# Kernel optimization log

Hardware: AMD Instinct MI355X
Metric: run time of the kernel (lower is better)

Reference implementation:

```python
import jax, jax.numpy as jnp
import numpy as np
from jax import lax


def setup_inputs() -> dict:
    key = jax.random.key(0)
    kx, kw = jax.random.split(key)
    x = jax.random.normal(kx, (32, 3, 8192), dtype=jnp.float32)
    weight = jax.random.normal(kw, (128, 3, 64), dtype=jnp.float32)
    return {"x": x, "weight": weight}


def reference(x, weight):
    # x: [B, C, L], weight: [O, C, K]
    K = weight.shape[2]
    # Cross-correlation (conv1d, no bias, valid padding): [B, O, L-K+1]
    conv_out = lax.conv_general_dilated(
        x, weight, window_strides=(1,), padding='VALID',
        dimension_numbers=('NCH', 'OIH', 'NCH'))
    # Half squared norm of each shapelet: [O]
    w_norm = jnp.sum(weight ** 2, axis=(1, 2)) / 2
    # Half squared norm of each length-K window, via cumulative sums
    # (avoids materializing the [B, C, W, K] unfold tensor)
    sq = jnp.sum(x ** 2, axis=1)               # [B, L]
    c = jnp.pad(jnp.cumsum(sq, axis=1), ((0, 0), (1, 0)))  # [B, L+1]
    win_norm = (c[:, K:] - c[:, :-K]) / 2      # [B, L-K+1]
    # features = conv_out - (||w||^2/2 + ||window||^2/2)
    features = conv_out - w_norm[None, :, None] - win_norm[:, None, :]
    # global max-pool over time, then *(-2) -> min squared distance
    return -2.0 * jnp.max(features, axis=-1)   # [B, O]
```

## Files before the change

kernel.cpp:

```cpp
#include <hip/hip_runtime.h>
#include <float.h>

#define BB 32
#define LL 8192
#define OO 128
#define KK 64
#define WW (LL - KK + 1)
#define TC 32

typedef __attribute__((ext_vector_type(8))) short short8;
typedef __attribute__((ext_vector_type(4))) float f32x4;

union AB { int4 i4; int i[4]; short8 v; };
union AB2 { struct { int4 a, b; } p; int i[8]; };

static __device__ __forceinline__ unsigned int f2bf(float f) {
    unsigned int u = __builtin_bit_cast(unsigned int, f);
    return (u + 0x7FFFu + ((u >> 16) & 1u)) >> 16;
}

__global__ __launch_bounds__(256) void prep_kernel(const float* __restrict__ w,
                                                   unsigned short* __restrict__ wswz,
                                                   float* __restrict__ wn) {
    int g = blockIdx.x * 256 + threadIdx.x;
    if (g < 3072) {
        int ob = (g >= 1536) ? 1 : 0;
        int gg = g - ob * 1536;
        int ksqp = gg >> 6;
        int o2   = gg & 63;
        int ks = ksqp >> 2, qp = ksqp & 3;
        int c = ks >> 1, h = ks & 1;
        const float4* p = (const float4*)(w + (ob * 64 + o2) * 192 + c * 64 + h * 32 + qp * 8);
        float4 v0 = p[0], v1 = p[1];
        int4 pk;
        pk.x = (int)(f2bf(v0.x) | (f2bf(v0.y) << 16));
        pk.y = (int)(f2bf(v0.z) | (f2bf(v0.w) << 16));
        pk.z = (int)(f2bf(v1.x) | (f2bf(v1.y) << 16));
        pk.w = (int)(f2bf(v1.z) | (f2bf(v1.w) << 16));
        ((int4*)wswz)[g] = pk;
    }
    int oo = g - 3072;
    if (oo >= 0 && oo < OO) {
        const float* p = w + oo * 192;
        float s = 0.f;
        for (int i = 0; i < 192; ++i) { float v = p[i]; s = fmaf(v, v, s); }
        wn[oo] = 0.5f * s;
    }
}

__global__ __launch_bounds__(256, 3) void shapeconv_main(const float* __restrict__ x,
                                                         const unsigned short* __restrict__ wswz,
                                                         const float* __restrict__ wn,
                                                         float* __restrict__ partial) {
    __shared__ __align__(16) unsigned short w_lds[64 * 192];
    __shared__ __align__(16) unsigned short x_lds[3 * 320];
    __shared__ float sq_lds[320];
    __shared__ float P_lds[40];
    __shared__ float win_lds[272];
    __shared__ float wn_lds[64];
    __shared__ float mred[64];

    const int tc = blockIdx.x;
    const int ob = blockIdx.y;
    const int b  = blockIdx.z;
    const int tid = threadIdx.x;
    const int wv = tid >> 6;
    const int lane = tid & 63;
    const int wo = wv & 1, wt = wv >> 1;
    const int n  = lane & 15;
    const int qp = lane >> 4;
    const int T0 = tc * 256;

    {
        const char* src = (const char*)(wswz + ob * 1536 * 8) + tid * 16;
        #pragma unroll
        for (int i = 0; i < 6; ++i) {
            __builtin_amdgcn_global_load_lds(
                (const __attribute__((address_space(1))) unsigned int*)(src + i * 4096),
                (__attribute__((address_space(3))) unsigned int*)((char*)w_lds + wv * 1024 + i * 4096),
                16, 0, 0);
        }
    }
    if (tid < 64) wn_lds[tid] = wn[ob * 64 + tid];

    if (tid < 240) {
        int c = tid / 80, j4 = tid - c * 80;
        int l = T0 + j4 * 4;
        float4 v = make_float4(0.f, 0.f, 0.f, 0.f);
        if (l < LL) v = *(const float4*)(x + (b * 3 + c) * LL + l);
        uint2 pk;
        pk.x = f2bf(v.x) | (f2bf(v.y) << 16);
        pk.y = f2bf(v.z) | (f2bf(v.w) << 16);
        *(uint2*)(x_lds + c * 320 + j4 * 4) = pk;
    }
    for (int j = tid; j < 320; j += 256) {
        int l = T0 + j;
        float s = 0.f;
        if (l < LL) {
            #pragma unroll
            for (int c = 0; c < 3; ++c) {
                float v = x[(b * 3 + c) * LL + l];
                s = fmaf(v, v, s);
            }
        }
        sq_lds[j] = s;
    }
    if (tid < 40) {
        float s = 0.f;
        #pragma unroll
        for (int k = 0; k < 8; ++k) {
            int l = T0 + tid * 8 + k;
            if (l < LL) {
                #pragma unroll
                for (int c = 0; c < 3; ++c) {
                    float v = x[(b * 3 + c) * LL + l];
                    s = fmaf(v, v, s);
                }
            }
        }
        P_lds[tid] = s;
    }
    __syncthreads();

    {
        int a = tid >> 3, bb2 = tid & 7;
        float s = 0.f;
        #pragma unroll
        for (int i = 1; i <= 7; ++i) s += P_lds[a + i];
        #pragma unroll
        for (int k = 0; k < 8; ++k)
            s += (k >= bb2) ? sq_lds[8 * a + k] : sq_lds[8 * a + 64 + k];
        int pi = tid + (tid >> 4);
        win_lds[pi] = (T0 + tid < WW) ? 0.5f * s : 1e30f;
    }
    __syncthreads();

    f32x4 acc[2][8];
    {
        float wl[8];
        #pragma unroll
        for (int r = 0; r < 8; ++r) {
            int tl = 128 * wt + r + 8 * n;
            wl[r] = win_lds[tl + (tl >> 4)];
        }
        #pragma unroll
        for (int ot = 0; ot < 2; ++ot)
            #pragma unroll
            for (int rg = 0; rg < 4; ++rg) {
                float nw = wn_lds[32 * wo + 16 * ot + 4 * qp + rg];
                #pragma unroll
                for (int r = 0; r < 8; ++r)
                    acc[ot][r][rg] = -nw - wl[r];
            }
    }

    const char* xb = (const char*)x_lds;
    #pragma unroll
    for (int ks = 0; ks < 6; ++ks) {
        int c = ks >> 1, h = ks & 1;
        int e0b = c * 640 + 256 * wt + 64 * h + 16 * (n + qp);
        AB2 D;
        D.p.a = *(const int4*)(xb + e0b);
        D.p.b = *(const int4*)(xb + e0b + 16);
        AB a0, a1;
        const int4* wq = (const int4*)w_lds + (ks * 4 + qp) * 64 + 32 * wo;
        a0.i4 = wq[n];
        a1.i4 = wq[16 + n];
        #pragma unroll
        for (int r = 0; r < 8; ++r) {
            AB bf;
            int s = r >> 1;
            if ((r & 1) == 0) {
                bf.i[0] = D.i[s]; bf.i[1] = D.i[s + 1]; bf.i[2] = D.i[s + 2]; bf.i[3] = D.i[s + 3];
            } else {
                #pragma unroll
                for (int d = 0; d < 4; ++d)
                    bf.i[d] = (int)(((unsigned)D.i[s + d] >> 16) | ((unsigned)D.i[s + d + 1] << 16));
            }
            acc[0][r] = __builtin_amdgcn_mfma_f32_16x16x32_bf16(a0.v, bf.v, acc[0][r], 0, 0, 0);
            acc[1][r] = __builtin_amdgcn_mfma_f32_16x16x32_bf16(a1.v, bf.v, acc[1][r], 0, 0, 0);
        }
    }

    float m2[2][4];
    #pragma unroll
    for (int ot = 0; ot < 2; ++ot)
        #pragma unroll
        for (int rg = 0; rg < 4; ++rg) {
            float mm = acc[ot][0][rg];
            #pragma unroll
            for (int r = 1; r < 8; ++r) mm = fmaxf(mm, acc[ot][r][rg]);
            m2[ot][rg] = mm;
        }
    #pragma unroll
    for (int s = 1; s <= 8; s <<= 1)
        #pragma unroll
        for (int ot = 0; ot < 2; ++ot)
            #pragma unroll
            for (int rg = 0; rg < 4; ++rg)
                m2[ot][rg] = fmaxf(m2[ot][rg], __shfl_xor(m2[ot][rg], s, 64));

    if (wt == 1 && n == 0) {
        #pragma unroll
        for (int ot = 0; ot < 2; ++ot)
            #pragma unroll
            for (int rg = 0; rg < 4; ++rg)
                mred[32 * wo + 16 * ot + 4 * qp + rg] = m2[ot][rg];
    }
    __syncthreads();
    if (wt == 0 && n == 0) {
        #pragma unroll
        for (int ot = 0; ot < 2; ++ot)
            #pragma unroll
            for (int rg = 0; rg < 4; ++rg) {
                int oi = 32 * wo + 16 * ot + 4 * qp + rg;
                float v = fmaxf(m2[ot][rg], mred[oi]);
                partial[((size_t)(b * TC + tc) * 2 + ob) * 64 + oi] = v;
            }
    }
}

__global__ __launch_bounds__(256) void reduce_kernel(const float* __restrict__ partial,
                                                     float* __restrict__ out) {
    int idx = blockIdx.x * 256 + threadIdx.x;
    int b = idx >> 7, o = idx & 127;
    const float* pp = partial + ((size_t)b * TC * 2 + (o >> 6)) * 64 + (o & 63);
    float mx = -FLT_MAX;
    #pragma unroll 8
    for (int tcc = 0; tcc < TC; ++tcc) mx = fmaxf(mx, pp[(size_t)tcc * 128]);
    out[idx] = -2.f * mx;
}

extern "C" void kernel_launch(void* const* d_in, const int* in_sizes, int n_in,
                              void* d_out, int out_size, void* d_ws, size_t ws_size,
                              hipStream_t stream) {
    const float* x = (const float*)d_in[0];
    const float* w = (const float*)d_in[1];
    float* out = (float*)d_out;

    unsigned short* wswz = (unsigned short*)d_ws;
    float* wn = (float*)((char*)d_ws + 49152);
    float* partial = (float*)((char*)d_ws + 49664);

    prep_kernel<<<13, 256, 0, stream>>>(w, wswz, wn);
    dim3 grid(TC, 2, BB);
    shapeconv_main<<<grid, 256, 0, stream>>>(x, wswz, wn, partial);
    reduce_kernel<<<16, 256, 0, stream>>>(partial, out);
}
```

Before: 82.64 us.

## Process four time chunks per block with double-buffered x staging

Each block now loops over four 256-sample time chunks instead of one. This amortizes the 24KB weight load into LDS across more work and cuts the grid from 2048 to 512 blocks. The next chunk's x data is staged into a second LDS buffer while the current chunk runs its MFMAs. The 8-sample partial sums are now computed with warp shuffles instead of redundant global reads. The risks are lower occupancy (launch bounds 2), fewer blocks to fill the GPU, and extra barriers per chunk.

```diff
diff --git a/kernel.cpp b/kernel.cpp
--- a/kernel.cpp
+++ b/kernel.cpp
@@ -6,13 +6,13 @@
 #define OO 128
 #define KK 64
 #define WW (LL - KK + 1)
-#define TC 32
+#define NCH 4
+#define GX 8
 
 typedef __attribute__((ext_vector_type(8))) short short8;
 typedef __attribute__((ext_vector_type(4))) float f32x4;
 
 union AB { int4 i4; int i[4]; short8 v; };
-union AB2 { struct { int4 a, b; } p; int i[8]; };
 
 static __device__ __forceinline__ unsigned int f2bf(float f) {
     unsigned int u = __builtin_bit_cast(unsigned int, f);
@@ -48,19 +48,66 @@
     }
 }
 
-__global__ __launch_bounds__(256, 3) void shapeconv_main(const float* __restrict__ x,
+static __device__ __forceinline__ void stage_chunk(const float* __restrict__ x, int b, int T0,
+                                                   unsigned short* xl, float* sql, float* Pl,
+                                                   int tid) {
+    if (tid < 240) {
+        int c = tid / 80, j4 = tid - c * 80;
+        int l = T0 + j4 * 4;
+        float4 v = make_float4(0.f, 0.f, 0.f, 0.f);
+        if (l < LL) v = *(const float4*)(x + (b * 3 + c) * LL + l);
+        uint2 pk;
+        pk.x = f2bf(v.x) | (f2bf(v.y) << 16);
+        pk.y = f2bf(v.z) | (f2bf(v.w) << 16);
+        *(uint2*)(xl + c * 320 + j4 * 4) = pk;
+    }
+    {
+        int l = T0 + tid;
+        float s = 0.f;
+        if (l < LL) {
+            #pragma unroll
+            for (int c = 0; c < 3; ++c) {
+                float v = x[(b * 3 + c) * LL + l];
+                s = fmaf(v, v, s);
+            }
+        }
+        sql[tid] = s;
+        float s8 = s + __shfl_xor(s, 1, 64);
+        s8 += __shfl_xor(s8, 2, 64);
+        s8 += __shfl_xor(s8, 4, 64);
+        if ((tid & 7) == 0) Pl[tid >> 3] = s8;
+    }
+    if (tid < 64) {
+        int j = 256 + tid, l = T0 + j;
+        float s = 0.f;
+        if (l < LL) {
+            #pragma unroll
+            for (int c = 0; c < 3; ++c) {
+                float v = x[(b * 3 + c) * LL + l];
+                s = fmaf(v, v, s);
+            }
+        }
+        sql[j] = s;
+        float s8 = s + __shfl_xor(s, 1, 64);
+        s8 += __shfl_xor(s8, 2, 64);
+        s8 += __shfl_xor(s8, 4, 64);
+        if ((tid & 7) == 0) Pl[32 + (tid >> 3)] = s8;
+    }
+}
+
+__global__ __launch_bounds__(256, 2) void shapeconv_main(const float* __restrict__ x,
                                                          const unsigned short* __restrict__ wswz,
                                                          const float* __restrict__ wn,
                                                          float* __restrict__ partial) {
     __shared__ __align__(16) unsigned short w_lds[64 * 192];
-    __shared__ __align__(16) unsigned short x_lds[3 * 320];
-    __shared__ float sq_lds[320];
-    __shared__ float P_lds[40];
+    __shared__ __align__(16) unsigned short x_lds[2][3 * 320];
+    __shared__ __align__(16) float sq_lds[2][320];
+    __shared__ float P_lds[2][40];
     __shared__ float win_lds[272];
     __shared__ float wn_lds[64];
     __shared__ float mred[64];
 
-    const int tc = blockIdx.x;
+    const int tcx = blockIdx.x;
     const int ob = blockIdx.y;
     const int b  = blockIdx.z;
     const int tid = threadIdx.x;
@@ -69,7 +116,7 @@
     const int wo = wv & 1, wt = wv >> 1;
     const int n  = lane & 15;
     const int qp = lane >> 4;
-    const int T0 = tc * 256;
+    const int Tb = tcx * (NCH * 256);
 
     {
         const char* src = (const char*)(wswz + ob * 1536 * 8) + tid * 16;
@@ -83,115 +130,95 @@
     }
     if (tid < 64) wn_lds[tid] = wn[ob * 64 + tid];
 
-    if (tid < 240) {
-        int c = tid / 80, j4 = tid - c * 80;
-        int l = T0 + j4 * 4;
-        float4 v = make_float4(0.f, 0.f, 0.f, 0.f);
-        if (l < LL) v = *(const float4*)(x + (b * 3 + c) * LL + l);
-        uint2 pk;
-        pk.x = f2bf(v.x) | (f2bf(v.y) << 16);
-        pk.y = f2bf(v.z) | (f2bf(v.w) << 16);
-        *(uint2*)(x_lds + c * 320 + j4 * 4) = pk;
-    }
-    for (int j = tid; j < 320; j += 256) {
-        int l = T0 + j;
-        float s = 0.f;
-        if (l < LL) {
-            #pragma unroll
-            for (int c = 0; c < 3; ++c) {
-                float v = x[(b * 3 + c) * LL + l];
-                s = fmaf(v, v, s);
-            }
-        }
-        sq_lds[j] = s;
-    }
-    if (tid < 40) {
-        float s = 0.f;
-        #pragma unroll
-        for (int k = 0; k < 8; ++k) {
-            int l = T0 + tid * 8 + k;
-            if (l < LL) {
-                #pragma unroll
-                for (int c = 0; c < 3; ++c) {
-                    float v = x[(b * 3 + c) * LL + l];
-                    s = fmaf(v, v, s);
-                }
-            }
-        }
-        P_lds[tid] = s;
-    }
-    __syncthreads();
-
-    {
-        int a = tid >> 3, bb2 = tid & 7;
-        float s = 0.f;
-        #pragma unroll
-        for (int i = 1; i <= 7; ++i) s += P_lds[a + i];
-        #pragma unroll
-        for (int k = 0; k < 8; ++k)
-            s += (k >= bb2) ? sq_lds[8 * a + k] : sq_lds[8 * a + 64 + k];
-        int pi = tid + (tid >> 4);
-        win_lds[pi] = (T0 + tid < WW) ? 0.5f * s : 1e30f;
-    }
-    __syncthreads();
-
-    f32x4 acc[2][8];
-    {
-        float wl[8];
-        #pragma unroll
-        for (int r = 0; r < 8; ++r) {
-            int tl = 128 * wt + r + 8 * n;
-            wl[r] = win_lds[tl + (tl >> 4)];
-        }
-        #pragma unroll
-        for (int ot = 0; ot < 2; ++ot)
-            #pragma unroll
-            for (int rg = 0; rg < 4; ++rg) {
-                float nw = wn_lds[32 * wo + 16 * ot + 4 * qp + rg];
-                #pragma unroll
-                for (int r = 0; r < 8; ++r)
-                    acc[ot][r][rg] = -nw - wl[r];
-            }
-    }
-
-    const char* xb = (const char*)x_lds;
-    #pragma unroll
-    for (int ks = 0; ks < 6; ++ks) {
-        int c = ks >> 1, h = ks & 1;
-        int e0b = c * 640 + 256 * wt + 64 * h + 16 * (n + qp);
-        AB2 D;
-        D.p.a = *(const int4*)(xb + e0b);
-        D.p.b = *(const int4*)(xb + e0b + 16);
-        AB a0, a1;
-        const int4* wq = (const int4*)w_lds + (ks * 4 + qp) * 64 + 32 * wo;
-        a0.i4 = wq[n];
-        a1.i4 = wq[16 + n];
-        #pragma unroll
-        for (int r = 0; r < 8; ++r) {
-            AB bf;
-            int s = r >> 1;
-            if ((r & 1) == 0) {
-                bf.i[0] = D.i[s]; bf.i[1] = D.i[s + 1]; bf.i[2] = D.i[s + 2]; bf.i[3] = D.i[s + 3];
-            } else {
-                #pragma unroll
-                for (int d = 0; d < 4; ++d)
-                    bf.i[d] = (int)(((unsigned)D.i[s + d] >> 16) | ((unsigned)D.i[s + d + 1] << 16));
-            }
-            acc[0][r] = __builtin_amdgcn_mfma_f32_16x16x32_bf16(a0.v, bf.v, acc[0][r], 0, 0, 0);
-            acc[1][r] = __builtin_amdgcn_mfma_f32_16x16x32_bf16(a1.v, bf.v, acc[1][r], 0, 0, 0);
-        }
-    }
+    stage_chunk(x, b, Tb, x_lds[0], sq_lds[0], P_lds[0], tid);
 
     float m2[2][4];
     #pragma unroll
     for (int ot = 0; ot < 2; ++ot)
         #pragma unroll
-        for (int rg = 0; rg < 4; ++rg) {
-            float mm = acc[ot][0][rg];
-            #pragma unroll
-            for (int r = 1; r < 8; ++r) mm = fmaxf(mm, acc[ot][r][rg]);
-            m2[ot][rg] = mm;
-        }
+        for (int rg = 0; rg < 4; ++rg) m2[ot][rg] = -FLT_MAX;
+
+    for (int ci = 0; ci < NCH; ++ci) {
+        const int bsel = ci & 1;
+        const int T0 = Tb + ci * 256;
+        __syncthreads();
+
+        {
+            int a = tid >> 3, bb2 = tid & 7;
+            const float* sql = sq_lds[bsel];
+            const float* Pl = P_lds[bsel];
+            float s = 0.f;
+            #pragma unroll
+            for (int i = 1; i <= 7; ++i) s += Pl[a + i];
+            #pragma unroll
+            for (int k = 0; k < 8; ++k)
+                s += (k >= bb2) ? sql[8 * a + k] : sql[8 * a + 64 + k];
+            int pi = tid + (tid >> 4);
+            win_lds[pi] = (T0 + tid < WW) ? 0.5f * s : 1e30f;
+        }
+        __syncthreads();
+
+        f32x4 acc[2][8];
+        {
+            float wl[8];
+            #pragma unroll
+            for (int r = 0; r < 8; ++r) {
+                int tl = 128 * wt + r + 8 * n;
+                wl[r] = win_lds[tl + (tl >> 4)];
+            }
+            #pragma unroll
+            for (int ot = 0; ot < 2; ++ot)
+                #pragma unroll
+                for (int rg = 0; rg < 4; ++rg) {
+                    float nw = wn_lds[32 * wo + 16 * ot + 4 * qp + rg];
+                    #pragma unroll
+                    for (int r = 0; r < 8; ++r)
+                        acc[ot][r][rg] = -nw - wl[r];
+                }
+        }
+
+        if (ci + 1 < NCH)
+            stage_chunk(x, b, T0 + 256, x_lds[1 - bsel], sq_lds[1 - bsel], P_lds[1 - bsel], tid);
+
+        const char* xb = (const char*)x_lds[bsel];
+        #pragma unroll
+        for (int ks = 0; ks < 6; ++ks) {
+            int c = ks >> 1, h = ks & 1;
+            int e0b = c * 640 + 256 * wt + 64 * h + 16 * (n + qp);
+            int4 Ea = *(const int4*)(xb + e0b);
+            int4 Eb = *(const int4*)(xb + e0b + 16);
+            int D[8] = {Ea.x, Ea.y, Ea.z, Ea.w, Eb.x, Eb.y, Eb.z, Eb.w};
+            AB a0, a1;
+            const int4* wq = (const int4*)w_lds + (ks * 4 + qp) * 64 + 32 * wo;
+            a0.i4 = wq[n];
+            a1.i4 = wq[16 + n];
+            #pragma unroll
+            for (int r = 0; r < 8; ++r) {
+                AB bf;
+                int s = r >> 1;
+                if ((r & 1) == 0) {
+                    bf.i[0] = D[s]; bf.i[1] = D[s + 1]; bf.i[2] = D[s + 2]; bf.i[3] = D[s + 3];
+                } else {
+                    #pragma unroll
+                    for (int d = 0; d < 4; ++d)
+                        bf.i[d] = (int)(((unsigned)D[s + d] >> 16) | ((unsigned)D[s + d + 1] << 16));
+                }
+                acc[0][r] = __builtin_amdgcn_mfma_f32_16x16x32_bf16(a0.v, bf.v, acc[0][r], 0, 0, 0);
+                acc[1][r] = __builtin_amdgcn_mfma_f32_16x16x32_bf16(a1.v, bf.v, acc[1][r], 0, 0, 0);
+            }
+        }
+
+        #pragma unroll
+        for (int ot = 0; ot < 2; ++ot)
+            #pragma unroll
+            for (int rg = 0; rg < 4; ++rg) {
+                float mm = m2[ot][rg];
+                #pragma unroll
+                for (int r = 0; r < 8; ++r) mm = fmaxf(mm, acc[ot][r][rg]);
+                m2[ot][rg] = mm;
+            }
+    }
+
     #pragma unroll
     for (int s = 1; s <= 8; s <<= 1)
         #pragma unroll
@@ -215,7 +242,7 @@
             for (int rg = 0; rg < 4; ++rg) {
                 int oi = 32 * wo + 16 * ot + 4 * qp + rg;
                 float v = fmaxf(m2[ot][rg], mred[oi]);
-                partial[((size_t)(b * TC + tc) * 2 + ob) * 64 + oi] = v;
+                partial[((size_t)(b * GX + tcx) * 2 + ob) * 64 + oi] = v;
             }
     }
 }
@@ -224,10 +251,10 @@
                                                      float* __restrict__ out) {
     int idx = blockIdx.x * 256 + threadIdx.x;
     int b = idx >> 7, o = idx & 127;
-    const float* pp = partial + ((size_t)b * TC * 2 + (o >> 6)) * 64 + (o & 63);
+    const float* pp = partial + ((size_t)b * GX * 2 + (o >> 6)) * 64 + (o & 63);
     float mx = -FLT_MAX;
-    #pragma unroll 8
-    for (int tcc = 0; tcc < TC; ++tcc) mx = fmaxf(mx, pp[(size_t)tcc * 128]);
+    #pragma unroll
+    for (int t = 0; t < GX; ++t) mx = fmaxf(mx, pp[(size_t)t * 128]);
     out[idx] = -2.f * mx;
 }
 
@@ -243,7 +270,7 @@
     float* partial = (float*)((char*)d_ws + 49664);
 
     prep_kernel<<<13, 256, 0, stream>>>(w, wswz, wn);
-    dim3 grid(TC, 2, BB);
+    dim3 grid(GX, 2, BB);
     shapeconv_main<<<grid, 256, 0, stream>>>(x, wswz, wn, partial);
     reduce_kernel<<<16, 256, 0, stream>>>(partial, out);
 }
```

After: 74.45 us. 1.11x faster.
